# Kernel tuning notes

Hardware: AMD Instinct MI355X
Metric: run time of the kernel (lower is better)

## Reference

```python
import jax, jax.numpy as jnp
import numpy as np

EPS = 1.01e-08
BN_EPS = 1e-5

def conv2d(x, w, b, stride, padding):
    y = jax.lax.conv_general_dilated(x, w, window_strides=stride, padding=padding,
                                     dimension_numbers=('NCHW', 'OIHW', 'NCHW'))
    return y + b[None, :, None, None]

def masknorm(x, mask, mask_norm):
    amp = jnp.sqrt(jnp.sum(x * x, axis=1, keepdims=True) + EPS)  # (B,1,F,T)
    if mask is None:
        return x / amp
    if mask_norm:
        mask_sum = jnp.sum(mask, axis=(2, 3), keepdims=True)
        return x * mask / (amp * mask_sum)
    return x * mask / amp

def flow_attention(q, k, v):
    # Flowformer linear attention, single head. q,k,v: (B, L, D)
    q = jax.nn.sigmoid(q)
    k = jax.nn.sigmoid(k)
    L = q.shape[1]
    sink_in = 1.0 / (jnp.einsum('bld,bd->bl', q + EPS, k.sum(1) + EPS))
    src_out = 1.0 / (jnp.einsum('bld,bd->bl', k + EPS, q.sum(1) + EPS))
    cons_sink = jnp.einsum('bld,bd->bl', q + EPS, (k * src_out[..., None]).sum(1) + EPS)
    cons_src = jnp.einsum('bld,bd->bl', k + EPS, (q * sink_in[..., None]).sum(1) + EPS)
    sink_alloc = jax.nn.sigmoid(cons_sink)
    src_comp = jax.nn.softmax(cons_src, axis=-1) * jnp.asarray(L, q.dtype)
    kv = jnp.einsum('bld,blm->bdm', k, v * src_comp[..., None])  # (B,D,D)
    out = jnp.einsum('bld,bdm->blm', q, kv) * sink_in[..., None] * sink_alloc[..., None]
    return out

def setup_inputs() -> dict:
    key = jax.random.key(0)
    ks = jax.random.split(key, 16)
    B, Cin, H, T = 4, 8, 252, 2048
    D = 12  # emb_dims
    inp = {
        'x': jax.random.normal(ks[0], (B, Cin, H, T), jnp.float32),
        'frame': jax.random.uniform(ks[1], (B, 1, 84, T), jnp.float32),
        # CBLR: Conv2d(8,16,5x5,same) + BatchNorm2d(16) + LeakyReLU
        'w_pre': jax.random.normal(ks[2], (16, 8, 5, 5), jnp.float32) * 0.05,
        'b_pre': jnp.zeros((16,), jnp.float32),
        'bn_gamma': jnp.ones((16,), jnp.float32),
        'bn_beta': jnp.zeros((16,), jnp.float32),
        'bn_mean': jnp.zeros((16,), jnp.float32),
        'bn_var': jnp.ones((16,), jnp.float32),
        'T': jnp.asarray(2.0, jnp.float32),
        'wq_conv': jax.random.normal(ks[3], (D, 16, 3, 3), jnp.float32) * 0.05,
        'bq_conv': jnp.zeros((D,), jnp.float32),
        'wkv_conv': jax.random.normal(ks[4], (D, 16, 3, 3), jnp.float32) * 0.05,
        'bkv_conv': jnp.zeros((D,), jnp.float32),
        # FlowAttention projections (single head, d_model = emb_dims = 12)
        'fa_wq': jax.random.normal(ks[5], (D, D), jnp.float32) * 0.3,
        'fa_bq': jnp.zeros((D,), jnp.float32),
        'fa_wk': jax.random.normal(ks[6], (D, D), jnp.float32) * 0.3,
        'fa_bk': jnp.zeros((D,), jnp.float32),
        'fa_wv': jax.random.normal(ks[7], (D, D), jnp.float32) * 0.3,
        'fa_bv': jnp.zeros((D,), jnp.float32),
        'fa_wo': jax.random.normal(ks[8], (D, D), jnp.float32) * 0.3,
        'fa_bo': jnp.zeros((D,), jnp.float32),
    }
    return inp

def reference(x, frame, w_pre, b_pre, bn_gamma, bn_beta, bn_mean, bn_var, T,
              wq_conv, bq_conv, wkv_conv, bkv_conv,
              fa_wq, fa_bq, fa_wk, fa_bk, fa_wv, fa_bv, fa_wo, fa_bo):
    # pre_encoding: Conv(same) -> BatchNorm(eval) -> LeakyReLU(0.01)
    h = conv2d(x, w_pre, b_pre, (1, 1), [(2, 2), (2, 2)])
    h = (h - bn_mean[None, :, None, None]) * jax.lax.rsqrt(bn_var + BN_EPS)[None, :, None, None]
    h = h * bn_gamma[None, :, None, None] + bn_beta[None, :, None, None]
    h = jnp.where(h >= 0, h, 0.01 * h)
    # embedding convs: kernel 3x3, stride (3,1), padding (0,1) -> (B,D,84,T)
    KV = conv2d(h, wkv_conv, bkv_conv, (3, 1), [(0, 0), (1, 1)])
    KV = masknorm(KV, frame, True) * T
    Q = conv2d(h, wq_conv, bq_conv, (3, 1), [(0, 0), (1, 1)])
    B, D, Fb, Tt = Q.shape
    # flatten spatial grid to a sequence of length L = F*T
    q = Q.reshape(B, D, Fb * Tt).transpose(0, 2, 1)
    kv = KV.reshape(B, D, Fb * Tt).transpose(0, 2, 1)
    qp = q @ fa_wq + fa_bq
    kp = kv @ fa_wk + fa_bk
    vp = kv @ fa_wv + fa_bv
    o = flow_attention(qp, kp, vp)
    o = o @ fa_wo + fa_bo  # dropout disabled (eval)
    emb = o.transpose(0, 2, 1).reshape(B, D, Fb, Tt)
    return emb
```

## Files before the change

kernel.cpp:

```cpp
#include <hip/hip_runtime.h>
#include <math.h>

#define EPSF 1.01e-08f

namespace {
constexpr int NB = 4;
constexpr int HH = 252, TW = 2048;
constexpr int C1 = 16, DD = 12, FF = 84;
constexpr int LLEN = FF * TW;

constexpr size_t OFF_H   = 0;
constexpr size_t SZ_H    = (size_t)NB * C1 * HH * TW;
constexpr size_t SZ_QKV  = (size_t)NB * LLEN * DD;
constexpr size_t OFF_Q   = OFF_H + SZ_H;
constexpr size_t OFF_K   = OFF_Q + SZ_QKV;
constexpr size_t OFF_V   = OFF_K + SZ_QKV;
constexpr size_t OFF_SI  = OFF_V + SZ_QKV;
constexpr size_t OFF_SA  = OFF_SI + (size_t)NB * LLEN;
constexpr size_t OFF_WP  = OFF_SA + (size_t)NB * LLEN;
constexpr size_t OFF_B1  = OFF_WP + 3200;
constexpr size_t OFF_WQT = OFF_B1 + 16;
constexpr size_t OFF_WKT = OFF_WQT + 1728;
constexpr size_t FTOT    = OFF_WKT + 1728;
constexpr size_t DBYTE   = FTOT * sizeof(float);

constexpr int DO_MSUM = 0;
constexpr int DO_KSUM = 4;
constexpr int DO_QSUM = 52;
constexpr int DO_SKQ  = 100;
constexpr int DO_SQS  = 148;
constexpr int DO_SE   = 196;
constexpr int DO_M    = 200;
constexpr int NDBL    = 776;
}

__device__ __forceinline__ float wsum(float v) {
#pragma unroll
  for (int m = 1; m < 64; m <<= 1) v += __shfl_xor(v, m, 64);
  return v;
}
__device__ __forceinline__ double wsumd(double v) {
#pragma unroll
  for (int m = 1; m < 64; m <<= 1) v += __shfl_xor(v, m, 64);
  return v;
}
__device__ __forceinline__ void atomAddD(double* p, double v) { unsafeAtomicAdd(p, v); }
__device__ __forceinline__ float sigm(float x) { return 1.f / (1.f + expf(-x)); }

__global__ void k_prep(const float* __restrict__ w_pre, const float* __restrict__ b_pre,
                       const float* __restrict__ g, const float* __restrict__ be,
                       const float* __restrict__ mean, const float* __restrict__ var,
                       const float* __restrict__ wq, const float* __restrict__ wkv,
                       float* __restrict__ ws) {
  int tid = blockIdx.x * 256 + threadIdx.x;
  int stride = gridDim.x * 256;
  if (tid < 16) {
    float sc = g[tid] / sqrtf(var[tid] + 1e-5f);
    ws[OFF_B1 + tid] = (b_pre[tid] - mean[tid]) * sc + be[tid];
  }
  for (int idx = tid; idx < 3200; idx += stride) {
    int co = idx & 15, r = idx >> 4;
    int ci = r / 25, p = r % 25;
    float sc = g[co] / sqrtf(var[co] + 1e-5f);
    ws[OFF_WP + idx] = w_pre[(co * 8 + ci) * 25 + p] * sc;
  }
  for (int idx = tid; idx < 1728; idx += stride) {
    int d = idx % 12, r = idx / 12;
    ws[OFF_WQT + idx] = wq[d * 144 + r];
    ws[OFF_WKT + idx] = wkv[d * 144 + r];
  }
}

__global__ __launch_bounds__(256, 3) void k_conv1(const float* __restrict__ x,
                                                  const float* __restrict__ wsc,
                                                  float* __restrict__ h) {
  __shared__ __align__(16) float wl[3200];
  __shared__ float bl[16];
  __shared__ __align__(16) float xs[6][544];

  const int cb = blockIdx.x * 512;
  const int y0 = blockIdx.y * 2;
  const int b = blockIdx.z;
  const int g = threadIdx.x >> 6;
  const int lane = threadIdx.x & 63;
  const int c0 = cb + lane * 8;

  for (int i = threadIdx.x * 4; i < 3200; i += 1024)
    *(float4*)(wl + i) = *(const float4*)(wsc + OFF_WP + i);
  if (threadIdx.x < 16) bl[threadIdx.x] = wsc[OFF_B1 + threadIdx.x];

  float acc[4][2][8];
#pragma unroll
  for (int co = 0; co < 4; co++)
#pragma unroll
    for (int r = 0; r < 2; r++)
#pragma unroll
      for (int j = 0; j < 8; j++) acc[co][r][j] = 0.f;

  for (int ci = 0; ci < 8; ci++) {
    __syncthreads();
    const float* xc = x + (size_t)(b * 8 + ci) * HH * TW;
    for (int li = threadIdx.x; li < 6 * 528; li += 256) {
      const int r = li / 528;
      const int c = li - r * 528;
      const int gy = y0 - 2 + r;
      const int gx = cb - 4 + c;
      float v = 0.f;
      if (gy >= 0 && gy < HH && gx >= 0 && gx < TW) v = xc[(size_t)gy * TW + gx];
      const int q = c >> 2;
      const int sq = q ^ ((q >> 3) & 7);
      xs[r][sq * 4 + (c & 3)] = v;
    }
    __syncthreads();

#pragma unroll
    for (int kh = 0; kh < 5; kh++) {
      float ra[16], rb[16];
#pragma unroll
      for (int k = 0; k < 4; k++) {
        const int q = lane * 2 + k;
        const int sq = q ^ ((q >> 3) & 7);
        *(float4*)(ra + 4 * k) = *(const float4*)(&xs[kh][sq * 4]);
        *(float4*)(rb + 4 * k) = *(const float4*)(&xs[kh + 1][sq * 4]);
      }
      const float* wrow = wl + (ci * 25 + kh * 5) * 16 + g * 4;
#pragma unroll
      for (int kw = 0; kw < 5; kw++) {
        const float4 w4 = *(const float4*)(wrow + kw * 16);
        const float wv[4] = {w4.x, w4.y, w4.z, w4.w};
#pragma unroll
        for (int co = 0; co < 4; co++)
#pragma unroll
          for (int j = 0; j < 8; j++) {
            acc[co][0][j] = fmaf(ra[2 + kw + j], wv[co], acc[co][0][j]);
            acc[co][1][j] = fmaf(rb[2 + kw + j], wv[co], acc[co][1][j]);
          }
      }
    }
  }

#pragma unroll
  for (int co = 0; co < 4; co++) {
    const float bb = bl[g * 4 + co];
    const size_t rowbase = (size_t)(b * 16 + g * 4 + co) * HH;
#pragma unroll
    for (int r = 0; r < 2; r++) {
      float4 o0, o1;
      float z;
      z = acc[co][r][0] + bb; o0.x = (z >= 0.f) ? z : 0.01f * z;
      z = acc[co][r][1] + bb; o0.y = (z >= 0.f) ? z : 0.01f * z;
      z = acc[co][r][2] + bb; o0.z = (z >= 0.f) ? z : 0.01f * z;
      z = acc[co][r][3] + bb; o0.w = (z >= 0.f) ? z : 0.01f * z;
      z = acc[co][r][4] + bb; o1.x = (z >= 0.f) ? z : 0.01f * z;
      z = acc[co][r][5] + bb; o1.y = (z >= 0.f) ? z : 0.01f * z;
      z = acc[co][r][6] + bb; o1.z = (z >= 0.f) ? z : 0.01f * z;
      z = acc[co][r][7] + bb; o1.w = (z >= 0.f) ? z : 0.01f * z;
      float* hp = h + (rowbase + (y0 + r)) * TW + c0;
      *(float4*)(hp) = o0;
      *(float4*)(hp + 4) = o1;
    }
  }
}

__global__ void k_masksum(const float* __restrict__ frame, double* __restrict__ dacc) {
  const int b = blockIdx.y;
  const float* fr = frame + (size_t)b * FF * TW;
  double s = 0.0;
  for (int i = blockIdx.x * 256 + threadIdx.x; i < FF * TW; i += gridDim.x * 256)
    s += (double)fr[i];
  s = wsumd(s);
  __shared__ double sm[4];
  int lane = threadIdx.x & 63, wid = threadIdx.x >> 6;
  if (lane == 0) sm[wid] = s;
  __syncthreads();
  if (threadIdx.x == 0) atomAddD(&dacc[DO_MSUM + b], sm[0] + sm[1] + sm[2] + sm[3]);
}

__global__ __launch_bounds__(256, 3) void k_conv2q(
    const float* __restrict__ h, const float* __restrict__ wsc,
    double* __restrict__ dacc,
    const float* __restrict__ fwq, const float* __restrict__ fbq,
    const float* __restrict__ bqc,
    float* __restrict__ qo) {
  const int c0 = (blockIdx.x * 256 + threadIdx.x) * 4;
  const int f = blockIdx.y;
  const int b = blockIdx.z;
  const bool interior = (c0 >= 4) && (c0 + 8 <= TW);

  float aq[12][4];
#pragma unroll
  for (int d = 0; d < 12; d++) {
    const float bq = bqc[d];
#pragma unroll
    for (int j = 0; j < 4; j++) aq[d][j] = bq;
  }

  for (int c = 0; c < 16; c++) {
    const float* hc = h + ((size_t)(b * 16 + c) * HH + 3 * f) * TW;
#pragma unroll
    for (int kh = 0; kh < 3; kh++) {
      const float* row = hc + (size_t)kh * TW;
      float xr[12];
      if (interior) {
#pragma unroll
        for (int v = 0; v < 3; v++)
          *(float4*)(xr + 4 * v) = *(const float4*)(row + c0 - 4 + 4 * v);
      } else {
#pragma unroll
        for (int j = 0; j < 12; j++) {
          int cc = c0 - 4 + j;
          xr[j] = (cc >= 0 && cc < TW) ? row[cc] : 0.f;
        }
      }
      const float* wp = wsc + OFF_WQT + (size_t)(c * 9 + kh * 3) * 12;
#pragma unroll
      for (int kw = 0; kw < 3; kw++) {
        const float4 w0 = *(const float4*)(wp + kw * 12);
        const float4 w1 = *(const float4*)(wp + kw * 12 + 4);
        const float4 w2 = *(const float4*)(wp + kw * 12 + 8);
        const float wv[12] = {w0.x, w0.y, w0.z, w0.w, w1.x, w1.y, w1.z, w1.w,
                              w2.x, w2.y, w2.z, w2.w};
#pragma unroll
        for (int j = 0; j < 4; j++) {
          const float xv = xr[3 + kw + j];
#pragma unroll
          for (int d = 0; d < 12; d++) aq[d][j] = fmaf(xv, wv[d], aq[d][j]);
        }
      }
    }
  }

  float s1[12][4];
#pragma unroll
  for (int d = 0; d < 12; d++) {
    const float bb = fbq[d];
#pragma unroll
    for (int j = 0; j < 4; j++) s1[d][j] = bb;
  }
#pragma unroll
  for (int e = 0; e < 12; e++) {
    const float4 w0 = *(const float4*)(fwq + e * 12);
    const float4 w1 = *(const float4*)(fwq + e * 12 + 4);
    const float4 w2 = *(const float4*)(fwq + e * 12 + 8);
    const float wv[12] = {w0.x, w0.y, w0.z, w0.w, w1.x, w1.y, w1.z, w1.w,
                          w2.x, w2.y, w2.z, w2.w};
#pragma unroll
    for (int j = 0; j < 4; j++) {
      const float a = aq[e][j];
#pragma unroll
      for (int d = 0; d < 12; d++) s1[d][j] = fmaf(a, wv[d], s1[d][j]);
    }
  }

  float qsumP[12];
#pragma unroll
  for (int d = 0; d < 12; d++) qsumP[d] = 0.f;
  const size_t lbase = (size_t)f * TW + c0;
#pragma unroll
  for (int j = 0; j < 4; j++) {
    const size_t o = ((size_t)b * LLEN + lbase + j) * 12;
#pragma unroll
    for (int d = 0; d < 12; d++) {
      const float qv = sigm(s1[d][j]);
      qsumP[d] += qv;
      qo[o + d] = qv;
    }
  }

  __shared__ float red[4 * 12];
  int lane = threadIdx.x & 63, wid = threadIdx.x >> 6;
#pragma unroll
  for (int d = 0; d < 12; d++) {
    float s = wsum(qsumP[d]);
    if (lane == 0) red[wid * 12 + d] = s;
  }
  __syncthreads();
  if (threadIdx.x < 12) {
    float tot = red[threadIdx.x] + red[12 + threadIdx.x] + red[24 + threadIdx.x] + red[36 + threadIdx.x];
    atomAddD(&dacc[DO_QSUM + b * 12 + threadIdx.x], (double)tot);
  }
}

__global__ __launch_bounds__(256, 3) void k_conv2kv(
    const float* __restrict__ h, const float* __restrict__ frame,
    const float* __restrict__ wsc, double* __restrict__ dacc,
    const float* __restrict__ fwk, const float* __restrict__ fbk,
    const float* __restrict__ fwv, const float* __restrict__ fbv,
    const float* __restrict__ bkvc, const float* __restrict__ Tp,
    float* __restrict__ ko, float* __restrict__ vo) {
  const int c0 = (blockIdx.x * 256 + threadIdx.x) * 4;
  const int f = blockIdx.y;
  const int b = blockIdx.z;
  const bool interior = (c0 >= 4) && (c0 + 8 <= TW);

  float akv[12][4];
#pragma unroll
  for (int d = 0; d < 12; d++) {
    const float bk = bkvc[d];
#pragma unroll
    for (int j = 0; j < 4; j++) akv[d][j] = bk;
  }

  for (int c = 0; c < 16; c++) {
    const float* hc = h + ((size_t)(b * 16 + c) * HH + 3 * f) * TW;
#pragma unroll
    for (int kh = 0; kh < 3; kh++) {
      const float* row = hc + (size_t)kh * TW;
      float xr[12];
      if (interior) {
#pragma unroll
        for (int v = 0; v < 3; v++)
          *(float4*)(xr + 4 * v) = *(const float4*)(row + c0 - 4 + 4 * v);
      } else {
#pragma unroll
        for (int j = 0; j < 12; j++) {
          int cc = c0 - 4 + j;
          xr[j] = (cc >= 0 && cc < TW) ? row[cc] : 0.f;
        }
      }
      const float* wp = wsc + OFF_WKT + (size_t)(c * 9 + kh * 3) * 12;
#pragma unroll
      for (int kw = 0; kw < 3; kw++) {
        const float4 w0 = *(const float4*)(wp + kw * 12);
        const float4 w1 = *(const float4*)(wp + kw * 12 + 4);
        const float4 w2 = *(const float4*)(wp + kw * 12 + 8);
        const float wv[12] = {w0.x, w0.y, w0.z, w0.w, w1.x, w1.y, w1.z, w1.w,
                              w2.x, w2.y, w2.z, w2.w};
#pragma unroll
        for (int j = 0; j < 4; j++) {
          const float xv = xr[3 + kw + j];
#pragma unroll
          for (int d = 0; d < 12; d++) akv[d][j] = fmaf(xv, wv[d], akv[d][j]);
        }
      }
    }
  }

  const float msum = (float)dacc[DO_MSUM + b];
  const float Tv = Tp[0];
  const float4 mk4 = *(const float4*)(frame + ((size_t)b * FF + f) * TW + c0);
  const float mks[4] = {mk4.x, mk4.y, mk4.z, mk4.w};
#pragma unroll
  for (int j = 0; j < 4; j++) {
    float ss = EPSF;
#pragma unroll
    for (int d = 0; d < 12; d++) ss = fmaf(akv[d][j], akv[d][j], ss);
    const float sc = mks[j] * Tv / (sqrtf(ss) * msum);
#pragma unroll
    for (int d = 0; d < 12; d++) akv[d][j] *= sc;
  }

  const size_t lbase = (size_t)f * TW + c0;
  float ksumP[12];
#pragma unroll
  for (int d = 0; d < 12; d++) ksumP[d] = 0.f;

  {
    float s2[12][4];
#pragma unroll
    for (int d = 0; d < 12; d++) {
      const float bb = fbk[d];
#pragma unroll
      for (int j = 0; j < 4; j++) s2[d][j] = bb;
    }
#pragma unroll
    for (int e = 0; e < 12; e++) {
      const float4 w0 = *(const float4*)(fwk + e * 12);
      const float4 w1 = *(const float4*)(fwk + e * 12 + 4);
      const float4 w2 = *(const float4*)(fwk + e * 12 + 8);
      const float wv[12] = {w0.x, w0.y, w0.z, w0.w, w1.x, w1.y, w1.z, w1.w,
                            w2.x, w2.y, w2.z, w2.w};
#pragma unroll
      for (int j = 0; j < 4; j++) {
        const float a = akv[e][j];
#pragma unroll
        for (int d = 0; d < 12; d++) s2[d][j] = fmaf(a, wv[d], s2[d][j]);
      }
    }
#pragma unroll
    for (int j = 0; j < 4; j++) {
      const size_t o = ((size_t)b * LLEN + lbase + j) * 12;
#pragma unroll
      for (int d = 0; d < 12; d++) {
        const float kk = sigm(s2[d][j]);
        ksumP[d] += kk;
        ko[o + d] = kk;
      }
    }
  }

  {
    float s3[12][4];
#pragma unroll
    for (int d = 0; d < 12; d++) {
      const float bb = fbv[d];
#pragma unroll
      for (int j = 0; j < 4; j++) s3[d][j] = bb;
    }
#pragma unroll
    for (int e = 0; e < 12; e++) {
      const float4 w0 = *(const float4*)(fwv + e * 12);
      const float4 w1 = *(const float4*)(fwv + e * 12 + 4);
      const float4 w2 = *(const float4*)(fwv + e * 12 + 8);
      const float wv[12] = {w0.x, w0.y, w0.z, w0.w, w1.x, w1.y, w1.z, w1.w,
                            w2.x, w2.y, w2.z, w2.w};
#pragma unroll
      for (int j = 0; j < 4; j++) {
        const float a = akv[e][j];
#pragma unroll
        for (int d = 0; d < 12; d++) s3[d][j] = fmaf(a, wv[d], s3[d][j]);
      }
    }
#pragma unroll
    for (int j = 0; j < 4; j++) {
      const size_t o = ((size_t)b * LLEN + lbase + j) * 12;
#pragma unroll
      for (int d = 0; d < 12; d++) vo[o + d] = s3[d][j];
    }
  }

  __shared__ float red[4 * 12];
  int lane = threadIdx.x & 63, wid = threadIdx.x >> 6;
#pragma unroll
  for (int d = 0; d < 12; d++) {
    float s = wsum(ksumP[d]);
    if (lane == 0) red[wid * 12 + d] = s;
  }
  __syncthreads();
  if (threadIdx.x < 12) {
    float tot = red[threadIdx.x] + red[12 + threadIdx.x] + red[24 + threadIdx.x] + red[36 + threadIdx.x];
    atomAddD(&dacc[DO_KSUM + b * 12 + threadIdx.x], (double)tot);
  }
}

__global__ __launch_bounds__(256) void k_sink(const float* __restrict__ q,
                                              const float* __restrict__ k,
                                              float* __restrict__ sink_in,
                                              double* __restrict__ dacc) {
  const int b = blockIdx.y;
  const int tid0 = blockIdx.x * 256 + threadIdx.x;
  float ksE[12], qsE[12];
#pragma unroll
  for (int d = 0; d < 12; d++) {
    ksE[d] = (float)(dacc[DO_KSUM + b * 12 + d] + (double)EPSF);
    qsE[d] = (float)(dacc[DO_QSUM + b * 12 + d] + (double)EPSF);
  }
  float askq[12], asqs[12];
#pragma unroll
  for (int d = 0; d < 12; d++) { askq[d] = 0.f; asqs[d] = 0.f; }
  for (int it = 0; it < 8; it++) {
    size_t l = (size_t)it * 21504 + tid0;
    const float* qp = q + ((size_t)b * LLEN + l) * 12;
    const float* kp = k + ((size_t)b * LLEN + l) * 12;
    float qv[12], kv[12];
#pragma unroll
    for (int d = 0; d < 12; d++) { qv[d] = qp[d]; kv[d] = kp[d]; }
    float s1 = 0.f, s2 = 0.f;
#pragma unroll
    for (int d = 0; d < 12; d++) {
      s1 = fmaf(qv[d] + EPSF, ksE[d], s1);
      s2 = fmaf(kv[d] + EPSF, qsE[d], s2);
    }
    float si = 1.f / s1;
    float so = 1.f / s2;
    sink_in[(size_t)b * LLEN + l] = si;
#pragma unroll
    for (int d = 0; d < 12; d++) {
      askq[d] = fmaf(kv[d], so, askq[d]);
      asqs[d] = fmaf(qv[d], si, asqs[d]);
    }
  }
  float part[24];
#pragma unroll
  for (int d = 0; d < 12; d++) { part[d] = askq[d]; part[12 + d] = asqs[d]; }
  __shared__ float red[4 * 24];
  int lane = threadIdx.x & 63, wid = threadIdx.x >> 6;
#pragma unroll
  for (int j = 0; j < 24; j++) {
    float s = wsum(part[j]);
    if (lane == 0) red[wid * 24 + j] = s;
  }
  __syncthreads();
  if (threadIdx.x < 24) {
    float tot = red[threadIdx.x] + red[24 + threadIdx.x] + red[48 + threadIdx.x] + red[72 + threadIdx.x];
    int idx = (threadIdx.x < 12) ? (DO_SKQ + b * 12 + threadIdx.x)
                                 : (DO_SQS + b * 12 + (threadIdx.x - 12));
    atomAddD(&dacc[idx], (double)tot);
  }
}

__global__ __launch_bounds__(256) void k_flow(const float* __restrict__ q,
                                              const float* __restrict__ k,
                                              const float* __restrict__ v,
                                              float* __restrict__ sink_alloc,
                                              double* __restrict__ dacc) {
  const int b = blockIdx.y;
  const int tid0 = blockIdx.x * 256 + threadIdx.x;
  float skqE[12], sqsE[12];
#pragma unroll
  for (int d = 0; d < 12; d++) {
    skqE[d] = (float)(dacc[DO_SKQ + b * 12 + d] + (double)EPSF);
    sqsE[d] = (float)(dacc[DO_SQS + b * 12 + d] + (double)EPSF);
  }
  float acc[144];
#pragma unroll
  for (int j = 0; j < 144; j++) acc[j] = 0.f;
  double se = 0.0;
  for (int it = 0; it < 4; it++) {
    size_t l = (size_t)it * 43008 + tid0;
    size_t o = ((size_t)b * LLEN + l) * 12;
    float qv[12], kv[12], vv[12];
#pragma unroll
    for (int d = 0; d < 12; d++) { qv[d] = q[o + d]; kv[d] = k[o + d]; vv[d] = v[o + d]; }
    float c1 = 0.f, c2 = 0.f;
#pragma unroll
    for (int d = 0; d < 12; d++) {
      c1 = fmaf(qv[d] + EPSF, skqE[d], c1);
      c2 = fmaf(kv[d] + EPSF, sqsE[d], c2);
    }
    sink_alloc[(size_t)b * LLEN + l] = sigm(c1);
    float e = expf(c2);
    se += (double)e;
#pragma unroll
    for (int d = 0; d < 12; d++) {
      float ke = kv[d] * e;
#pragma unroll
      for (int m = 0; m < 12; m++) acc[d * 12 + m] = fmaf(ke, vv[m], acc[d * 12 + m]);
    }
  }
  __shared__ float red[4 * 144];
  __shared__ double seds[4];
  int lane = threadIdx.x & 63, wid = threadIdx.x >> 6;
#pragma unroll
  for (int j = 0; j < 144; j++) {
    float s = wsum(acc[j]);
    if (lane == 0) red[wid * 144 + j] = s;
  }
  double sew = wsumd(se);
  if (lane == 0) seds[wid] = sew;
  __syncthreads();
  if (threadIdx.x < 144) {
    float tot = red[threadIdx.x] + red[144 + threadIdx.x] + red[288 + threadIdx.x] + red[432 + threadIdx.x];
    atomAddD(&dacc[DO_M + b * 144 + threadIdx.x], (double)tot);
  }
  if (threadIdx.x == 192) atomAddD(&dacc[DO_SE + b], seds[0] + seds[1] + seds[2] + seds[3]);
}

__global__ __launch_bounds__(256) void k_out(const float* __restrict__ q,
                                             const float* __restrict__ sink_in,
                                             const float* __restrict__ sink_alloc,
                                             const double* __restrict__ dacc,
                                             const float* __restrict__ wo,
                                             const float* __restrict__ bo,
                                             float* __restrict__ out) {
  const int t = blockIdx.x * 256 + threadIdx.x;
  const int f = blockIdx.y;
  const int b = blockIdx.z;
  __shared__ float kvf[144];
  if (threadIdx.x < 144) {
    double fac = (double)LLEN / dacc[DO_SE + b];
    kvf[threadIdx.x] = (float)(dacc[DO_M + b * 144 + threadIdx.x] * fac);
  }
  __syncthreads();
  size_t l = (size_t)f * TW + t;
  const float* qp = q + ((size_t)b * LLEN + l) * 12;
  float qv[12];
#pragma unroll
  for (int d = 0; d < 12; d++) qv[d] = qp[d];
  float s = sink_in[(size_t)b * LLEN + l] * sink_alloc[(size_t)b * LLEN + l];
  float o[12];
#pragma unroll
  for (int m = 0; m < 12; m++) {
    float a = 0.f;
#pragma unroll
    for (int d = 0; d < 12; d++) a = fmaf(qv[d], kvf[d * 12 + m], a);
    o[m] = a * s;
  }
#pragma unroll
  for (int m2 = 0; m2 < 12; m2++) {
    float a = bo[m2];
#pragma unroll
    for (int m = 0; m < 12; m++) a = fmaf(o[m], wo[m * 12 + m2], a);
    out[((size_t)b * 12 + m2) * LLEN + l] = a;
  }
}

extern "C" void kernel_launch(void* const* d_in, const int* in_sizes, int n_in,
                              void* d_out, int out_size, void* d_ws, size_t ws_size,
                              hipStream_t stream) {
  (void)in_sizes; (void)n_in; (void)out_size; (void)ws_size;
  const float* x     = (const float*)d_in[0];
  const float* frame = (const float*)d_in[1];
  const float* w_pre = (const float*)d_in[2];
  const float* b_pre = (const float*)d_in[3];
  const float* gam   = (const float*)d_in[4];
  const float* bet   = (const float*)d_in[5];
  const float* mean  = (const float*)d_in[6];
  const float* var   = (const float*)d_in[7];
  const float* Tp    = (const float*)d_in[8];
  const float* wq_c  = (const float*)d_in[9];
  const float* bq_c  = (const float*)d_in[10];
  const float* wkv_c = (const float*)d_in[11];
  const float* bkv_c = (const float*)d_in[12];
  const float* fa_wq = (const float*)d_in[13];
  const float* fa_bq = (const float*)d_in[14];
  const float* fa_wk = (const float*)d_in[15];
  const float* fa_bk = (const float*)d_in[16];
  const float* fa_wv = (const float*)d_in[17];
  const float* fa_bv = (const float*)d_in[18];
  const float* fa_wo = (const float*)d_in[19];
  const float* fa_bo = (const float*)d_in[20];

  float* ws = (float*)d_ws;
  double* dacc = (double*)((char*)d_ws + DBYTE);
  float* out = (float*)d_out;

  hipMemsetAsync(dacc, 0, NDBL * sizeof(double), stream);
  k_prep<<<dim3(16), 256, 0, stream>>>(w_pre, b_pre, gam, bet, mean, var, wq_c, wkv_c, ws);
  k_masksum<<<dim3(64, 4), 256, 0, stream>>>(frame, dacc);
  k_conv1<<<dim3(4, 126, 4), 256, 0, stream>>>(x, ws, ws + OFF_H);
  k_conv2q<<<dim3(2, 84, 4), 256, 0, stream>>>(ws + OFF_H, ws, dacc,
      fa_wq, fa_bq, bq_c, ws + OFF_Q);
  k_conv2kv<<<dim3(2, 84, 4), 256, 0, stream>>>(ws + OFF_H, frame, ws, dacc,
      fa_wk, fa_bk, fa_wv, fa_bv, bkv_c, Tp, ws + OFF_K, ws + OFF_V);
  k_sink<<<dim3(84, 4), 256, 0, stream>>>(ws + OFF_Q, ws + OFF_K, ws + OFF_SI, dacc);
  k_flow<<<dim3(168, 4), 256, 0, stream>>>(ws + OFF_Q, ws + OFF_K, ws + OFF_V, ws + OFF_SA, dacc);
  k_out<<<dim3(8, 84, 4), 256, 0, stream>>>(ws + OFF_Q, ws + OFF_SI, ws + OFF_SA, dacc,
      fa_wo, fa_bo, out);
}
```

Baseline: 646.4 us.

## Load conv1 input rows straight from global memory into registers, drop the LDS tile

```diff
diff --git a/kernel.cpp b/kernel.cpp
--- a/kernel.cpp
+++ b/kernel.cpp
@@ -71,72 +71,82 @@
   }
 }
 
-__global__ __launch_bounds__(256, 3) void k_conv1(const float* __restrict__ x,
+#define C1_FMA(orow, W)                                         \
+  _Pragma("unroll")                                             \
+  for (int kw = 0; kw < 5; kw++) {                              \
+    const float4 w4 = W[kw];                                    \
+    _Pragma("unroll")                                           \
+    for (int j = 0; j < 4; j++) {                               \
+      const float xv = xr[j + kw + 2];                          \
+      acc[0][orow][j] = fmaf(xv, w4.x, acc[0][orow][j]);        \
+      acc[1][orow][j] = fmaf(xv, w4.y, acc[1][orow][j]);        \
+      acc[2][orow][j] = fmaf(xv, w4.z, acc[2][orow][j]);        \
+      acc[3][orow][j] = fmaf(xv, w4.w, acc[3][orow][j]);        \
+    }                                                           \
+  }
+
+#define C1_LOADROW(R) {                                         \
+    const int gy = y0 - 2 + (R);                                \
+    const bool gyok = (gy >= 0) && (gy < HH);                   \
+    const float* rp = xc + (size_t)gy * TW;                     \
+    _Pragma("unroll")                                           \
+    for (int k = 0; k < 3; k++) {                               \
+      const int gx = c0 - 4 + 4 * k;                            \
+      float4 v = make_float4(0.f, 0.f, 0.f, 0.f);               \
+      if (gyok && gx >= 0 && gx + 4 <= TW)                      \
+        v = *(const float4*)(rp + gx);                          \
+      *(float4*)(xr + 4 * k) = v;                               \
+    }                                                           \
+  }
+
+__global__ __launch_bounds__(256, 4) void k_conv1(const float* __restrict__ x,
                                                   const float* __restrict__ wsc,
                                                   float* __restrict__ h) {
   __shared__ __align__(16) float wl[3200];
   __shared__ float bl[16];
-  __shared__ __align__(16) float xs[6][544];
-
-  const int cb = blockIdx.x * 512;
+
+  const int cb = blockIdx.x * 256;
   const int y0 = blockIdx.y * 2;
   const int b = blockIdx.z;
   const int g = threadIdx.x >> 6;
   const int lane = threadIdx.x & 63;
-  const int c0 = cb + lane * 8;
+  const int c0 = cb + lane * 4;
 
   for (int i = threadIdx.x * 4; i < 3200; i += 1024)
     *(float4*)(wl + i) = *(const float4*)(wsc + OFF_WP + i);
   if (threadIdx.x < 16) bl[threadIdx.x] = wsc[OFF_B1 + threadIdx.x];
-
-  float acc[4][2][8];
+  __syncthreads();
+
+  float acc[4][2][4];
 #pragma unroll
   for (int co = 0; co < 4; co++)
 #pragma unroll
     for (int r = 0; r < 2; r++)
 #pragma unroll
-      for (int j = 0; j < 8; j++) acc[co][r][j] = 0.f;
+      for (int j = 0; j < 4; j++) acc[co][r][j] = 0.f;
 
   for (int ci = 0; ci < 8; ci++) {
-    __syncthreads();
     const float* xc = x + (size_t)(b * 8 + ci) * HH * TW;
-    for (int li = threadIdx.x; li < 6 * 528; li += 256) {
-      const int r = li / 528;
-      const int c = li - r * 528;
-      const int gy = y0 - 2 + r;
-      const int gx = cb - 4 + c;
-      float v = 0.f;
-      if (gy >= 0 && gy < HH && gx >= 0 && gx < TW) v = xc[(size_t)gy * TW + gx];
-      const int q = c >> 2;
-      const int sq = q ^ ((q >> 3) & 7);
-      xs[r][sq * 4 + (c & 3)] = v;
-    }
-    __syncthreads();
-
-#pragma unroll
-    for (int kh = 0; kh < 5; kh++) {
-      float ra[16], rb[16];
-#pragma unroll
-      for (int k = 0; k < 4; k++) {
-        const int q = lane * 2 + k;
-        const int sq = q ^ ((q >> 3) & 7);
-        *(float4*)(ra + 4 * k) = *(const float4*)(&xs[kh][sq * 4]);
-        *(float4*)(rb + 4 * k) = *(const float4*)(&xs[kh + 1][sq * 4]);
-      }
-      const float* wrow = wl + (ci * 25 + kh * 5) * 16 + g * 4;
-#pragma unroll
-      for (int kw = 0; kw < 5; kw++) {
-        const float4 w4 = *(const float4*)(wrow + kw * 16);
-        const float wv[4] = {w4.x, w4.y, w4.z, w4.w};
-#pragma unroll
-        for (int co = 0; co < 4; co++)
-#pragma unroll
-          for (int j = 0; j < 8; j++) {
-            acc[co][0][j] = fmaf(ra[2 + kw + j], wv[co], acc[co][0][j]);
-            acc[co][1][j] = fmaf(rb[2 + kw + j], wv[co], acc[co][1][j]);
-          }
-      }
-    }
+    float4 wA[5], wB[5];
+#pragma unroll
+    for (int kw = 0; kw < 5; kw++)
+      wA[kw] = *(const float4*)(wl + (ci * 25 + kw) * 16 + g * 4);
+    float xr[12];
+    C1_LOADROW(0);
+    C1_FMA(0, wA)
+#pragma unroll
+    for (int r = 1; r <= 4; r++) {
+#pragma unroll
+      for (int kw = 0; kw < 5; kw++)
+        wB[kw] = *(const float4*)(wl + (ci * 25 + r * 5 + kw) * 16 + g * 4);
+      C1_LOADROW(r);
+      C1_FMA(0, wB)
+      C1_FMA(1, wA)
+#pragma unroll
+      for (int kw = 0; kw < 5; kw++) wA[kw] = wB[kw];
+    }
+    C1_LOADROW(5);
+    C1_FMA(1, wA)
   }
 
 #pragma unroll
@@ -145,19 +155,13 @@
     const size_t rowbase = (size_t)(b * 16 + g * 4 + co) * HH;
 #pragma unroll
     for (int r = 0; r < 2; r++) {
-      float4 o0, o1;
+      float4 o;
       float z;
-      z = acc[co][r][0] + bb; o0.x = (z >= 0.f) ? z : 0.01f * z;
-      z = acc[co][r][1] + bb; o0.y = (z >= 0.f) ? z : 0.01f * z;
-      z = acc[co][r][2] + bb; o0.z = (z >= 0.f) ? z : 0.01f * z;
-      z = acc[co][r][3] + bb; o0.w = (z >= 0.f) ? z : 0.01f * z;
-      z = acc[co][r][4] + bb; o1.x = (z >= 0.f) ? z : 0.01f * z;
-      z = acc[co][r][5] + bb; o1.y = (z >= 0.f) ? z : 0.01f * z;
-      z = acc[co][r][6] + bb; o1.z = (z >= 0.f) ? z : 0.01f * z;
-      z = acc[co][r][7] + bb; o1.w = (z >= 0.f) ? z : 0.01f * z;
-      float* hp = h + (rowbase + (y0 + r)) * TW + c0;
-      *(float4*)(hp) = o0;
-      *(float4*)(hp + 4) = o1;
+      z = acc[co][r][0] + bb; o.x = (z >= 0.f) ? z : 0.01f * z;
+      z = acc[co][r][1] + bb; o.y = (z >= 0.f) ? z : 0.01f * z;
+      z = acc[co][r][2] + bb; o.z = (z >= 0.f) ? z : 0.01f * z;
+      z = acc[co][r][3] + bb; o.w = (z >= 0.f) ? z : 0.01f * z;
+      *(float4*)(h + (rowbase + (y0 + r)) * TW + c0) = o;
     }
   }
 }
@@ -618,7 +622,7 @@
   hipMemsetAsync(dacc, 0, NDBL * sizeof(double), stream);
   k_prep<<<dim3(16), 256, 0, stream>>>(w_pre, b_pre, gam, bet, mean, var, wq_c, wkv_c, ws);
   k_masksum<<<dim3(64, 4), 256, 0, stream>>>(frame, dacc);
-  k_conv1<<<dim3(4, 126, 4), 256, 0, stream>>>(x, ws, ws + OFF_H);
+  k_conv1<<<dim3(8, 126, 4), 256, 0, stream>>>(x, ws, ws + OFF_H);
   k_conv2q<<<dim3(2, 84, 4), 256, 0, stream>>>(ws + OFF_H, ws, dacc,
       fa_wq, fa_bq, bq_c, ws + OFF_Q);
   k_conv2kv<<<dim3(2, 84, 4), 256, 0, stream>>>(ws + OFF_H, frame, ws, dacc,
```

New measurement: 1.476 ms. 2.28x slower.
